# Optimization experiments

Measured on AMD Instinct MI355X. Metric: run time of the kernel, lower is better.

## Reference

```python
import jax, jax.numpy as jnp
import numpy as np

B = 2048
F = 267          # frame_size
L = 32           # latent_size
H = 256          # hidden_size (hard-coded in module)
E = 8            # num_experts
G = 64           # gate hidden size (hard-coded)
IN0 = L + F      # decoder layer0 input (latent + frame*cond_frames)
IN1 = L + H      # decoder inter input
OUT = F          # num_future_predictions * frame_size


def _lin_init(key, out_dim, in_dim):
    # kaiming-uniform-like scale
    bound = float(np.sqrt(1.0 / in_dim))
    return jax.random.uniform(key, (out_dim, in_dim), jnp.float32, -bound, bound)


def setup_inputs() -> dict:
    key = jax.random.key(0)
    ks = jax.random.split(key, 24)
    d = {}
    d["x"] = jax.random.normal(ks[0], (B, F), jnp.float32)
    d["c"] = jax.random.normal(ks[1], (B, F), jnp.float32)
    # encoder
    d["fc1_w"] = _lin_init(ks[2], H, 2 * F); d["fc1_b"] = jnp.zeros((H,), jnp.float32)
    d["fc2_w"] = _lin_init(ks[3], H, F + H); d["fc2_b"] = jnp.zeros((H,), jnp.float32)
    d["mu_w"] = _lin_init(ks[4], L, F + H);  d["mu_b"] = jnp.zeros((L,), jnp.float32)
    d["lv_w"] = _lin_init(ks[5], L, F + H);  d["lv_b"] = jnp.zeros((L,), jnp.float32)
    # gate
    d["g0_w"] = _lin_init(ks[6], G, IN0); d["g0_b"] = jnp.zeros((G,), jnp.float32)
    d["g1_w"] = _lin_init(ks[7], G, G);   d["g1_b"] = jnp.zeros((G,), jnp.float32)
    d["g2_w"] = _lin_init(ks[8], E, G);   d["g2_b"] = jnp.zeros((E,), jnp.float32)
    # expert weights [E, in, out], biases [E, out], bias filled 0.01 as in module
    d["w0"] = jax.random.uniform(ks[9], (E, IN0, H), jnp.float32, -1, 1) * np.sqrt(1.0 / IN0)
    d["b0"] = jnp.full((E, H), 0.01, jnp.float32)
    d["w1"] = jax.random.uniform(ks[10], (E, IN1, H), jnp.float32, -1, 1) * np.sqrt(1.0 / IN1)
    d["b1"] = jnp.full((E, H), 0.01, jnp.float32)
    d["w2"] = jax.random.uniform(ks[11], (E, IN1, OUT), jnp.float32, -1, 1) * np.sqrt(1.0 / IN1)
    d["b2"] = jnp.full((E, OUT), 0.01, jnp.float32)
    return d


def reference(x, c, fc1_w, fc1_b, fc2_w, fc2_b, mu_w, mu_b, lv_w, lv_b,
              g0_w, g0_b, g1_w, g1_b, g2_w, g2_b, w0, b0, w1, b1, w2, b2):
    elu = jax.nn.elu
    # ---- encoder ----
    h1 = elu(jnp.concatenate([x, c], axis=1) @ fc1_w.T + fc1_b)
    h2 = elu(jnp.concatenate([x, h1], axis=1) @ fc2_w.T + fc2_b)
    s = jnp.concatenate([x, h2], axis=1)
    mu = s @ mu_w.T + mu_b
    logvar = s @ lv_w.T + lv_b
    eps = jax.random.normal(jax.random.key(42), mu.shape, mu.dtype)
    z = mu + eps * jnp.exp(0.5 * logvar)
    # ---- mixed decoder ----
    g = elu(jnp.concatenate([z, c], axis=1) @ g0_w.T + g0_b)
    g = elu(g @ g1_w.T + g1_b)
    coeff = jax.nn.softmax(g @ g2_w.T + g2_b, axis=1)  # [B, E]
    layer_out = c
    for (W, bvec, act) in ((w0, b0, True), (w1, b1, True), (w2, b2, False)):
        inp = jnp.concatenate([z, layer_out], axis=1)          # [B, in]
        # per-expert GEMM then coefficient mixing (same math as per-sample
        # mixed-weight bmm: coeff @ flat_weight then baddbmm)
        out = jnp.einsum('be,bi,eio->bo', coeff, inp, W, optimize=True)
        out = out + coeff @ bvec                               # mixed bias
        layer_out = elu(out) if act else out
    return (layer_out, mu, logvar)
```

## Files before the change

### kernel.cpp

```cpp
#include <hip/hip_runtime.h>
#include <math.h>
#include <stdint.h>

#define DI __device__ __forceinline__

typedef __attribute__((ext_vector_type(8))) short bf16x8;
typedef __attribute__((ext_vector_type(4))) float f32x4;
typedef __attribute__((ext_vector_type(4))) int i32x4;

DI float elu_f(float v) { return v > 0.f ? v : expm1f(v); }

DI unsigned short f2bf(float f) {
  uint32_t u = __float_as_uint(f);
  return (unsigned short)((u + 0x7FFFu + ((u >> 16) & 1u)) >> 16);
}

DI void threefry2x32(uint32_t k0, uint32_t k1, uint32_t& x0, uint32_t& x1) {
  uint32_t ks0 = k0, ks1 = k1, ks2 = k0 ^ k1 ^ 0x1BD11BDAu;
  x0 += ks0; x1 += ks1;
#define TFR(r) { x0 += x1; x1 = (x1 << r) | (x1 >> (32 - r)); x1 ^= x0; }
  TFR(13) TFR(15) TFR(26) TFR(6)   x0 += ks1; x1 += ks2 + 1u;
  TFR(17) TFR(29) TFR(16) TFR(24)  x0 += ks2; x1 += ks0 + 2u;
  TFR(13) TFR(15) TFR(26) TFR(6)   x0 += ks0; x1 += ks1 + 3u;
  TFR(17) TFR(29) TFR(16) TFR(24)  x0 += ks1; x1 += ks2 + 4u;
  TFR(13) TFR(15) TFR(26) TFR(6)   x0 += ks2; x1 += ks0 + 5u;
#undef TFR
}

DI float erfinv_f(float x) {
  float w = -logf((1.0f - x) * (1.0f + x));
  float p;
  if (w < 5.0f) {
    w -= 2.5f;
    p = 2.81022636e-08f;
    p = fmaf(p, w, 3.43273939e-07f);
    p = fmaf(p, w, -3.5233877e-06f);
    p = fmaf(p, w, -4.39150654e-06f);
    p = fmaf(p, w, 0.00021858087f);
    p = fmaf(p, w, -0.00125372503f);
    p = fmaf(p, w, -0.00417768164f);
    p = fmaf(p, w, 0.246640727f);
    p = fmaf(p, w, 1.50140941f);
  } else {
    w = sqrtf(w) - 3.0f;
    p = -0.000200214257f;
    p = fmaf(p, w, 0.000100950558f);
    p = fmaf(p, w, 0.00134934322f);
    p = fmaf(p, w, -0.00367342844f);
    p = fmaf(p, w, 0.00573950773f);
    p = fmaf(p, w, -0.0076224613f);
    p = fmaf(p, w, 0.00943887047f);
    p = fmaf(p, w, 1.00167406f);
    p = fmaf(p, w, 2.83297682f);
  }
  return p * x;
}

struct MegaArgs {
  const float *x, *c;
  const float *fc1w, *fc1b, *fc2w, *fc2b, *muw, *mub, *lvw, *lvb;
  const float *g0w, *g0b, *g1w, *g1b, *g2w, *g2b;
  const float *w0, *b0, *w1, *b1, *w2, *b2;
  unsigned short *Ax, *Axh, *Axh2, *A0, *A1, *A2;
  unsigned short *fc1t, *fc2t, *mlvt, *g0t, *g1t, *w0b, *w1b, *w2b;
  float *cf, *outY, *outMu, *outLv;
};

template <int KT, int NE, int D, bool ELU, bool OUTF32>
__global__ __launch_bounds__(128, 2)
void pipe32(const unsigned short* __restrict__ A,
            const unsigned short* __restrict__ Wt, int N,
            const float* __restrict__ bias,
            const float* __restrict__ cfp,
            unsigned short* __restrict__ Cb, int ldcb, int cb_off,
            float* __restrict__ Cf) {
  constexpr int Kp = KT * 32, TT = NE * KT;
  __shared__ float bias_s[NE * 32];
  __shared__ float cfs[(NE > 1) ? 256 : 1];
  const int tid = threadIdx.x, lane = tid & 63, wv = tid >> 6;
  const int q = lane >> 4, l16 = lane & 15;
  const int m0 = blockIdx.x * 32;
  const int n0 = blockIdx.y * 32 + wv * 16;
  const int gc = n0 + l16;
  const int wrow = (gc < N) ? gc : (N - 1);
  const unsigned short* wlane = Wt + (size_t)wrow * Kp + q * 8;

  bf16x8 ring[D];
#pragma unroll
  for (int g = 0; g < D; g++) {
    if (g < TT) {
      int e = g / KT, c = g % KT;
      ring[g] = *(const bf16x8*)(wlane + (size_t)e * N * Kp + c * 32);
    }
  }
  bf16x8 areg[2][KT];
#pragma unroll
  for (int t = 0; t < 2; t++) {
    const unsigned short* alane = A + (size_t)(m0 + t * 16 + l16) * Kp + q * 8;
#pragma unroll
    for (int c = 0; c < KT; c++) areg[t][c] = *(const bf16x8*)(alane + c * 32);
  }

  if (NE == 1) {
    if (tid < 32) {
      int col = blockIdx.y * 32 + tid;
      bias_s[tid] = (col < N) ? bias[col] : 0.f;
    }
  } else {
    for (int idx = tid; idx < NE * 32; idx += 128) {
      int e = idx >> 5, col = blockIdx.y * 32 + (idx & 31);
      bias_s[idx] = (col < N) ? bias[(size_t)e * N + col] : 0.f;
    }
    for (int idx = tid; idx < 256; idx += 128)
      cfs[idx] = cfp[(size_t)(m0 + (idx >> 3)) * 8 + (idx & 7)];
  }
  __syncthreads();

  f32x4 acc[2] = {{0.f, 0.f, 0.f, 0.f}, {0.f, 0.f, 0.f, 0.f}};
  f32x4 accF[2] = {{0.f, 0.f, 0.f, 0.f}, {0.f, 0.f, 0.f, 0.f}};
#pragma unroll
  for (int g = 0; g < TT; g++) {
    const int e = g / KT, c = g % KT;
    bf16x8 bv = ring[g % D];
    acc[0] = __builtin_amdgcn_mfma_f32_16x16x32_bf16(areg[0][c], bv, acc[0], 0, 0, 0);
    acc[1] = __builtin_amdgcn_mfma_f32_16x16x32_bf16(areg[1][c], bv, acc[1], 0, 0, 0);
    if (g + D < TT) {
      int e2 = (g + D) / KT, c2 = (g + D) % KT;
      ring[g % D] = *(const bf16x8*)(wlane + (size_t)e2 * N * Kp + c2 * 32);
    }
    if (NE > 1 && c == KT - 1) {
      float bv2 = bias_s[e * 32 + wv * 16 + l16];
#pragma unroll
      for (int t = 0; t < 2; t++)
#pragma unroll
        for (int r = 0; r < 4; r++) {
          float ce = cfs[(t * 16 + q * 4 + r) * 8 + e];
          accF[t][r] += ce * (acc[t][r] + bv2);
          acc[t][r] = 0.f;
        }
    }
  }

  if (gc < N) {
#pragma unroll
    for (int t = 0; t < 2; t++)
#pragma unroll
      for (int r = 0; r < 4; r++) {
        int row = m0 + t * 16 + q * 4 + r;
        float v = (NE > 1) ? accF[t][r] : (acc[t][r] + bias_s[wv * 16 + l16]);
        if (ELU) v = elu_f(v);
        if (OUTF32) Cf[(size_t)row * 267 + gc] = v;
        else Cb[(size_t)row * ldcb + cb_off + gc] = f2bf(v);
      }
  }
}

__global__ __launch_bounds__(256) void k_prep(MegaArgs a) {
  __shared__ __align__(16) unsigned short T[64][72];
  const int bb = blockIdx.x, tid = threadIdx.x;
  if (bb < 512) {
    for (int rr = 0; rr < 4; rr++) {
      int b = bb * 4 + rr;
      const float* xr = a.x + (size_t)b * 267;
      const float* cr = a.c + (size_t)b * 267;
      unsigned short* axr = a.Ax + (size_t)b * 544;
      for (int k = tid; k < 544; k += 256) {
        float v = (k < 267) ? xr[k] : ((k < 534) ? cr[k - 267] : 0.f);
        axr[k] = f2bf(v);
      }
      unsigned short* ahr = a.Axh + (size_t)b * 544;
      unsigned short* ah2 = a.Axh2 + (size_t)b * 544;
      for (int k = tid; k < 267; k += 256) { unsigned short v = f2bf(xr[k]); ahr[k] = v; ah2[k] = v; }
      for (int k = 523 + tid; k < 544; k += 256) { ahr[k] = 0; ah2[k] = 0; }
      unsigned short* a0r = a.A0 + (size_t)b * 320;
      for (int k = tid; k < 288; k += 256)
        a0r[32 + k] = (k < 267) ? f2bf(cr[k]) : (unsigned short)0;
    }
  } else if (bb < 1152) {
    int r = bb - 512;
    const float* src; unsigned short* dst; int Ks, Kp2;
    if (r < 256)      { src = a.fc1w + (size_t)r * 534; dst = a.fc1t + (size_t)r * 544; Ks = 534; Kp2 = 544; }
    else if (r < 512) { int n = r - 256; src = a.fc2w + (size_t)n * 523; dst = a.fc2t + (size_t)n * 544; Ks = 523; Kp2 = 544; }
    else if (r < 576) { int n = r - 512; src = (n < 32) ? (a.muw + (size_t)n * 523) : (a.lvw + (size_t)(n - 32) * 523);
                        dst = a.mlvt + (size_t)n * 544; Ks = 523; Kp2 = 544; }
    else              { int n = r - 576; src = a.g0w + (size_t)n * 299; dst = a.g0t + (size_t)n * 320; Ks = 299; Kp2 = 320; }
    for (int k = tid; k < Kp2; k += 256) dst[k] = (k < Ks) ? f2bf(src[k]) : (unsigned short)0;
  } else if (bb == 1152) {
    for (int k = tid; k < 4096; k += 256) a.g1t[k] = f2bf(a.g1w[k]);
  } else {
    int t = bb - 1153;
    const float* W; unsigned short* D; int K, N2, Kp2, ldW, e, kt, nt;
    if (t < 160)      { e = t / 20;  int lt = t % 20;  kt = lt / 4; nt = lt % 4; W = a.w0; D = a.w0b; K = 299; N2 = 256; Kp2 = 320; ldW = 256; }
    else if (t < 320) { int u = t - 160; e = u / 20; int lt = u % 20; kt = lt / 4; nt = lt % 4; W = a.w1; D = a.w1b; K = 288; N2 = 256; Kp2 = 288; ldW = 256; }
    else              { int u = t - 320; e = u / 25; int lt = u % 25; kt = lt / 5; nt = lt % 5; W = a.w2; D = a.w2b; K = 288; N2 = 267; Kp2 = 288; ldW = 267; }
    const int k0 = kt * 64, n0 = nt * 64;
    const float* We = W + (size_t)e * K * ldW;
    const int jj = tid & 63, ii0 = tid >> 6;
#pragma unroll
    for (int p = 0; p < 16; p++) {
      int i = ii0 + p * 4;
      int gk = k0 + i, gn = n0 + jj;
      float v = (gk < K && gn < N2) ? We[(size_t)gk * ldW + gn] : 0.f;
      T[jj][i] = f2bf(v);
    }
    __syncthreads();
    int j = tid >> 2, chb = tid & 3;
    int gn = n0 + j;
    if (gn < N2) {
      unsigned short* drow = D + ((size_t)e * N2 + gn) * Kp2 + k0;
#pragma unroll
      for (int s = 0; s < 2; s++) {
        int ch = chb + s * 4;
        if (k0 + ch * 8 < Kp2) {
          i32x4 v = *(i32x4*)(&T[j][ch * 8]);
          *(i32x4*)(drow + ch * 8) = v;
        }
      }
    }
  }
}

__global__ __launch_bounds__(256, 2) void k_mulv_gate(MegaArgs a) {
  __shared__ float mlvS[16 * 65];
  __shared__ __align__(16) unsigned short A0p[16 * 328];
  __shared__ __align__(16) unsigned short gaB[16 * 72];
  __shared__ __align__(16) unsigned short g1B[64 * 72];
  __shared__ float g2wT[64 * 8];
  __shared__ float gB[16 * 65];
  __shared__ float lg[16 * 8];
  const int tid = threadIdx.x, lane = tid & 63, wid = tid >> 6;
  const int q = lane >> 4, l16 = lane & 15;
  const int m0 = blockIdx.x * 16;
  const int cl = wid * 16 + l16;

  const unsigned short* alane = a.Axh2 + (size_t)(m0 + l16) * 544 + q * 8;
  const unsigned short* wlA = a.mlvt + (size_t)cl * 544 + q * 8;
  bf16x8 ring[8];
#pragma unroll
  for (int g = 0; g < 8; g++) ring[g] = *(const bf16x8*)(wlA + g * 32);
  bf16x8 areg[17];
#pragma unroll
  for (int c = 0; c < 17; c++) areg[c] = *(const bf16x8*)(alane + c * 32);
  f32x4 acc = {0.f, 0.f, 0.f, 0.f};
#pragma unroll
  for (int g = 0; g < 17; g++) {
    acc = __builtin_amdgcn_mfma_f32_16x16x32_bf16(areg[g], ring[g % 8], acc, 0, 0, 0);
    if (g + 8 < 17) ring[g % 8] = *(const bf16x8*)(wlA + (g + 8) * 32);
  }
#pragma unroll
  for (int r = 0; r < 4; r++) mlvS[(q * 4 + r) * 65 + cl] = acc[r];
  for (int idx = tid; idx < 576; idx += 256) {
    int row = idx / 36, ch = 4 + idx % 36;
    *(i32x4*)(A0p + row * 328 + ch * 8) =
        *(const i32x4*)(a.A0 + (size_t)(m0 + row) * 320 + ch * 8);
  }
  if (tid < 16) { i32x4 z4 = {0, 0, 0, 0}; *(i32x4*)(A0p + tid * 328 + 320) = z4; }
  for (int idx = tid; idx < 512; idx += 256) {
    int row = idx >> 3, ch = idx & 7;
    *(i32x4*)(g1B + row * 72 + ch * 8) = *(const i32x4*)(a.g1t + (size_t)row * 64 + ch * 8);
  }
  for (int idx = tid; idx < 512; idx += 256)
    g2wT[(idx & 63) * 8 + (idx >> 6)] = a.g2w[idx];
  __syncthreads();

  {
    const int m = tid >> 4, j0 = (tid & 15) * 2, R = m0 + m;
#pragma unroll
    for (int jj = 0; jj < 2; jj++) {
      int j = j0 + jj;
      float mu = mlvS[m * 65 + j] + a.mub[j];
      float lvv = mlvS[m * 65 + j + 32] + a.lvb[j];
      uint32_t x0 = 0u, x1 = (uint32_t)(R * 32 + j);
      threefry2x32(0u, 42u, x0, x1);
      uint32_t bits = x0 ^ x1;
      float f = __uint_as_float((bits >> 9) | 0x3F800000u) - 1.0f;
      const float lo = -0.99999994039535522461f;
      float u = fmaf(f, 2.0f, lo);
      u = fmaxf(u, lo);
      float eps = 1.41421356237f * erfinv_f(u);
      float z = fmaf(eps, expf(0.5f * lvv), mu);
      a.outMu[(size_t)R * 32 + j] = mu;
      a.outLv[(size_t)R * 32 + j] = lvv;
      unsigned short zb = f2bf(z);
      A0p[m * 328 + j] = zb;
      a.A0[(size_t)R * 320 + j] = zb;
      a.A1[(size_t)R * 288 + j] = zb;
      a.A2[(size_t)R * 288 + j] = zb;
    }
  }
  __syncthreads();

  const unsigned short* wlC = a.g0t + (size_t)cl * 320 + q * 8;
  bf16x8 ring2[8];
#pragma unroll
  for (int g = 0; g < 8; g++) ring2[g] = *(const bf16x8*)(wlC + g * 32);
  f32x4 accC = {0.f, 0.f, 0.f, 0.f};
#pragma unroll
  for (int g = 0; g < 10; g++) {
    bf16x8 av = *(const bf16x8*)(A0p + l16 * 328 + g * 32 + q * 8);
    accC = __builtin_amdgcn_mfma_f32_16x16x32_bf16(av, ring2[g % 8], accC, 0, 0, 0);
    if (g + 8 < 10) ring2[g % 8] = *(const bf16x8*)(wlC + (g + 8) * 32);
  }
  {
    float bc = a.g0b[cl];
#pragma unroll
    for (int r = 0; r < 4; r++)
      gaB[(q * 4 + r) * 72 + cl] = f2bf(elu_f(accC[r] + bc));
  }
  __syncthreads();

  f32x4 accD = {0.f, 0.f, 0.f, 0.f};
#pragma unroll
  for (int tau = 0; tau < 2; tau++) {
    bf16x8 av = *(const bf16x8*)(gaB + l16 * 72 + tau * 32 + q * 8);
    bf16x8 bv = *(const bf16x8*)(g1B + cl * 72 + tau * 32 + q * 8);
    accD = __builtin_amdgcn_mfma_f32_16x16x32_bf16(av, bv, accD, 0, 0, 0);
  }
  {
    float bc = a.g1b[cl];
#pragma unroll
    for (int r = 0; r < 4; r++)
      gB[(q * 4 + r) * 65 + cl] = elu_f(accD[r] + bc);
  }
  __syncthreads();

  if (tid < 128) {
    int r = tid >> 3, e = tid & 7;
    float d = a.g2b[e];
#pragma unroll 8
    for (int k = 0; k < 64; k++) d = fmaf(gB[r * 65 + k], g2wT[k * 8 + e], d);
    lg[r * 8 + e] = d;
  }
  __syncthreads();
  if (tid < 16) {
    float mx = lg[tid * 8];
#pragma unroll
    for (int e2 = 1; e2 < 8; e2++) mx = fmaxf(mx, lg[tid * 8 + e2]);
    float s = 0.f, ex[8];
#pragma unroll
    for (int e2 = 0; e2 < 8; e2++) { ex[e2] = expf(lg[tid * 8 + e2] - mx); s += ex[e2]; }
    float inv = 1.f / s;
#pragma unroll
    for (int e2 = 0; e2 < 8; e2++) a.cf[(size_t)(m0 + tid) * 8 + e2] = ex[e2] * inv;
  }
}

extern "C" void kernel_launch(void* const* d_in, const int* in_sizes, int n_in,
                              void* d_out, int out_size, void* d_ws, size_t ws_size,
                              hipStream_t stream) {
  (void)in_sizes; (void)n_in; (void)out_size; (void)ws_size;
  float* out = (float*)d_out;
  float* ws = (float*)d_ws;

  MegaArgs a;
  a.x    = (const float*)d_in[0];
  a.c    = (const float*)d_in[1];
  a.fc1w = (const float*)d_in[2];  a.fc1b = (const float*)d_in[3];
  a.fc2w = (const float*)d_in[4];  a.fc2b = (const float*)d_in[5];
  a.muw  = (const float*)d_in[6];  a.mub  = (const float*)d_in[7];
  a.lvw  = (const float*)d_in[8];  a.lvb  = (const float*)d_in[9];
  a.g0w  = (const float*)d_in[10]; a.g0b  = (const float*)d_in[11];
  a.g1w  = (const float*)d_in[12]; a.g1b  = (const float*)d_in[13];
  a.g2w  = (const float*)d_in[14]; a.g2b  = (const float*)d_in[15];
  a.w0   = (const float*)d_in[16]; a.b0   = (const float*)d_in[17];
  a.w1   = (const float*)d_in[18]; a.b1   = (const float*)d_in[19];
  a.w2   = (const float*)d_in[20]; a.b2   = (const float*)d_in[21];

  a.outY  = out;
  a.outMu = out + 2048 * 267;
  a.outLv = a.outMu + 2048 * 32;

  a.Ax   = (unsigned short*)(ws);
  a.Axh  = (unsigned short*)(ws + 557056);
  a.Axh2 = (unsigned short*)(ws + 1114112);
  a.A0   = (unsigned short*)(ws + 1671168);
  a.A1   = (unsigned short*)(ws + 1998848);
  a.A2   = (unsigned short*)(ws + 2293760);
  a.fc1t = (unsigned short*)(ws + 2588672);
  a.fc2t = (unsigned short*)(ws + 2658304);
  a.mlvt = (unsigned short*)(ws + 2727936);
  a.g0t  = (unsigned short*)(ws + 2745344);
  a.g1t  = (unsigned short*)(ws + 2755584);
  a.w0b  = (unsigned short*)(ws + 2757632);
  a.w1b  = (unsigned short*)(ws + 3085312);
  a.w2b  = (unsigned short*)(ws + 3380224);
  a.cf   = ws + 3687808;

  dim3 blkP(256), blkG(128);
  k_prep<<<1673, blkP, 0, stream>>>(a);
  pipe32<17, 1, 12, true, false><<<dim3(64, 8), blkG, 0, stream>>>(
      a.Ax, a.fc1t, 256, a.fc1b, nullptr, a.Axh, 544, 267, nullptr);
  pipe32<17, 1, 12, true, false><<<dim3(64, 8), blkG, 0, stream>>>(
      a.Axh, a.fc2t, 256, a.fc2b, nullptr, a.Axh2, 544, 267, nullptr);
  k_mulv_gate<<<128, blkP, 0, stream>>>(a);
  pipe32<10, 8, 12, true, false><<<dim3(64, 8), blkG, 0, stream>>>(
      a.A0, a.w0b, 256, a.b0, a.cf, a.A1, 288, 32, nullptr);
  pipe32<9, 8, 12, true, false><<<dim3(64, 8), blkG, 0, stream>>>(
      a.A1, a.w1b, 256, a.b1, a.cf, a.A2, 288, 32, nullptr);
  pipe32<9, 8, 12, false, true><<<dim3(64, 9), blkG, 0, stream>>>(
      a.A2, a.w2b, 267, a.b2, a.cf, nullptr, 0, 0, a.outY);
}
```

Measured before the change: 175.8 us.

## Fuse prep into encoder GEMMs and convert fp32 weights to bf16 on the fly

Removes the separate prep kernel. The first encoder GEMM now loads x/c fp32 rows directly into LDS as bf16 and writes the x part of the next activation buffer. The expert weight transposes run as extra blocks of that same launch. Encoder, mu/logvar and gate GEMMs read fp32 weights directly and pack them to bf16 in registers, which removes the transposed-weight buffers and one launch. The cost is more global fp32 weight traffic per block, with strided per-lane scalar loads and redundant conversion work in every block.

```diff
diff --git a/kernel.cpp b/kernel.cpp
--- a/kernel.cpp
+++ b/kernel.cpp
@@ -8,11 +8,20 @@
 typedef __attribute__((ext_vector_type(4))) float f32x4;
 typedef __attribute__((ext_vector_type(4))) int i32x4;
 
+#define MFMA16(av, bv, acc) __builtin_amdgcn_mfma_f32_16x16x32_bf16(av, bv, acc, 0, 0, 0)
+
 DI float elu_f(float v) { return v > 0.f ? v : expm1f(v); }
 
 DI unsigned short f2bf(float f) {
   uint32_t u = __float_as_uint(f);
   return (unsigned short)((u + 0x7FFFu + ((u >> 16) & 1u)) >> 16);
+}
+
+DI bf16x8 pack8(const float (&v)[8]) {
+  bf16x8 o;
+#pragma unroll
+  for (int j = 0; j < 8; j++) o[j] = (short)f2bf(v[j]);
+  return o;
 }
 
 DI void threefry2x32(uint32_t k0, uint32_t k1, uint32_t& x0, uint32_t& x1) {
@@ -61,150 +70,33 @@
   const float *fc1w, *fc1b, *fc2w, *fc2b, *muw, *mub, *lvw, *lvb;
   const float *g0w, *g0b, *g1w, *g1b, *g2w, *g2b;
   const float *w0, *b0, *w1, *b1, *w2, *b2;
-  unsigned short *Ax, *Axh, *Axh2, *A0, *A1, *A2;
-  unsigned short *fc1t, *fc2t, *mlvt, *g0t, *g1t, *w0b, *w1b, *w2b;
+  unsigned short *Axh, *Axh2, *A0, *A1, *A2;
+  unsigned short *w0b, *w1b, *w2b;
   float *cf, *outY, *outMu, *outLv;
 };
 
-template <int KT, int NE, int D, bool ELU, bool OUTF32>
-__global__ __launch_bounds__(128, 2)
-void pipe32(const unsigned short* __restrict__ A,
-            const unsigned short* __restrict__ Wt, int N,
-            const float* __restrict__ bias,
-            const float* __restrict__ cfp,
-            unsigned short* __restrict__ Cb, int ldcb, int cb_off,
-            float* __restrict__ Cf) {
-  constexpr int Kp = KT * 32, TT = NE * KT;
-  __shared__ float bias_s[NE * 32];
-  __shared__ float cfs[(NE > 1) ? 256 : 1];
-  const int tid = threadIdx.x, lane = tid & 63, wv = tid >> 6;
-  const int q = lane >> 4, l16 = lane & 15;
-  const int m0 = blockIdx.x * 32;
-  const int n0 = blockIdx.y * 32 + wv * 16;
-  const int gc = n0 + l16;
-  const int wrow = (gc < N) ? gc : (N - 1);
-  const unsigned short* wlane = Wt + (size_t)wrow * Kp + q * 8;
-
-  bf16x8 ring[D];
-#pragma unroll
-  for (int g = 0; g < D; g++) {
-    if (g < TT) {
-      int e = g / KT, c = g % KT;
-      ring[g] = *(const bf16x8*)(wlane + (size_t)e * N * Kp + c * 32);
-    }
-  }
-  bf16x8 areg[2][KT];
-#pragma unroll
-  for (int t = 0; t < 2; t++) {
-    const unsigned short* alane = A + (size_t)(m0 + t * 16 + l16) * Kp + q * 8;
-#pragma unroll
-    for (int c = 0; c < KT; c++) areg[t][c] = *(const bf16x8*)(alane + c * 32);
-  }
-
-  if (NE == 1) {
-    if (tid < 32) {
-      int col = blockIdx.y * 32 + tid;
-      bias_s[tid] = (col < N) ? bias[col] : 0.f;
-    }
-  } else {
-    for (int idx = tid; idx < NE * 32; idx += 128) {
-      int e = idx >> 5, col = blockIdx.y * 32 + (idx & 31);
-      bias_s[idx] = (col < N) ? bias[(size_t)e * N + col] : 0.f;
-    }
-    for (int idx = tid; idx < 256; idx += 128)
-      cfs[idx] = cfp[(size_t)(m0 + (idx >> 3)) * 8 + (idx & 7)];
-  }
-  __syncthreads();
-
-  f32x4 acc[2] = {{0.f, 0.f, 0.f, 0.f}, {0.f, 0.f, 0.f, 0.f}};
-  f32x4 accF[2] = {{0.f, 0.f, 0.f, 0.f}, {0.f, 0.f, 0.f, 0.f}};
-#pragma unroll
-  for (int g = 0; g < TT; g++) {
-    const int e = g / KT, c = g % KT;
-    bf16x8 bv = ring[g % D];
-    acc[0] = __builtin_amdgcn_mfma_f32_16x16x32_bf16(areg[0][c], bv, acc[0], 0, 0, 0);
-    acc[1] = __builtin_amdgcn_mfma_f32_16x16x32_bf16(areg[1][c], bv, acc[1], 0, 0, 0);
-    if (g + D < TT) {
-      int e2 = (g + D) / KT, c2 = (g + D) % KT;
-      ring[g % D] = *(const bf16x8*)(wlane + (size_t)e2 * N * Kp + c2 * 32);
-    }
-    if (NE > 1 && c == KT - 1) {
-      float bv2 = bias_s[e * 32 + wv * 16 + l16];
-#pragma unroll
-      for (int t = 0; t < 2; t++)
-#pragma unroll
-        for (int r = 0; r < 4; r++) {
-          float ce = cfs[(t * 16 + q * 4 + r) * 8 + e];
-          accF[t][r] += ce * (acc[t][r] + bv2);
-          acc[t][r] = 0.f;
-        }
-    }
-  }
-
-  if (gc < N) {
-#pragma unroll
-    for (int t = 0; t < 2; t++)
-#pragma unroll
-      for (int r = 0; r < 4; r++) {
-        int row = m0 + t * 16 + q * 4 + r;
-        float v = (NE > 1) ? accF[t][r] : (acc[t][r] + bias_s[wv * 16 + l16]);
-        if (ELU) v = elu_f(v);
-        if (OUTF32) Cf[(size_t)row * 267 + gc] = v;
-        else Cb[(size_t)row * ldcb + cb_off + gc] = f2bf(v);
-      }
-  }
-}
-
-__global__ __launch_bounds__(256) void k_prep(MegaArgs a) {
-  __shared__ __align__(16) unsigned short T[64][72];
-  const int bb = blockIdx.x, tid = threadIdx.x;
-  if (bb < 512) {
-    for (int rr = 0; rr < 4; rr++) {
-      int b = bb * 4 + rr;
-      const float* xr = a.x + (size_t)b * 267;
-      const float* cr = a.c + (size_t)b * 267;
-      unsigned short* axr = a.Ax + (size_t)b * 544;
-      for (int k = tid; k < 544; k += 256) {
-        float v = (k < 267) ? xr[k] : ((k < 534) ? cr[k - 267] : 0.f);
-        axr[k] = f2bf(v);
-      }
-      unsigned short* ahr = a.Axh + (size_t)b * 544;
-      unsigned short* ah2 = a.Axh2 + (size_t)b * 544;
-      for (int k = tid; k < 267; k += 256) { unsigned short v = f2bf(xr[k]); ahr[k] = v; ah2[k] = v; }
-      for (int k = 523 + tid; k < 544; k += 256) { ahr[k] = 0; ah2[k] = 0; }
-      unsigned short* a0r = a.A0 + (size_t)b * 320;
-      for (int k = tid; k < 288; k += 256)
-        a0r[32 + k] = (k < 267) ? f2bf(cr[k]) : (unsigned short)0;
-    }
-  } else if (bb < 1152) {
-    int r = bb - 512;
-    const float* src; unsigned short* dst; int Ks, Kp2;
-    if (r < 256)      { src = a.fc1w + (size_t)r * 534; dst = a.fc1t + (size_t)r * 544; Ks = 534; Kp2 = 544; }
-    else if (r < 512) { int n = r - 256; src = a.fc2w + (size_t)n * 523; dst = a.fc2t + (size_t)n * 544; Ks = 523; Kp2 = 544; }
-    else if (r < 576) { int n = r - 512; src = (n < 32) ? (a.muw + (size_t)n * 523) : (a.lvw + (size_t)(n - 32) * 523);
-                        dst = a.mlvt + (size_t)n * 544; Ks = 523; Kp2 = 544; }
-    else              { int n = r - 576; src = a.g0w + (size_t)n * 299; dst = a.g0t + (size_t)n * 320; Ks = 299; Kp2 = 320; }
-    for (int k = tid; k < Kp2; k += 256) dst[k] = (k < Ks) ? f2bf(src[k]) : (unsigned short)0;
-  } else if (bb == 1152) {
-    for (int k = tid; k < 4096; k += 256) a.g1t[k] = f2bf(a.g1w[k]);
-  } else {
-    int t = bb - 1153;
-    const float* W; unsigned short* D; int K, N2, Kp2, ldW, e, kt, nt;
-    if (t < 160)      { e = t / 20;  int lt = t % 20;  kt = lt / 4; nt = lt % 4; W = a.w0; D = a.w0b; K = 299; N2 = 256; Kp2 = 320; ldW = 256; }
-    else if (t < 320) { int u = t - 160; e = u / 20; int lt = u % 20; kt = lt / 4; nt = lt % 4; W = a.w1; D = a.w1b; K = 288; N2 = 256; Kp2 = 288; ldW = 256; }
-    else              { int u = t - 320; e = u / 25; int lt = u % 25; kt = lt / 5; nt = lt % 5; W = a.w2; D = a.w2b; K = 288; N2 = 267; Kp2 = 288; ldW = 267; }
-    const int k0 = kt * 64, n0 = nt * 64;
-    const float* We = W + (size_t)e * K * ldW;
-    const int jj = tid & 63, ii0 = tid >> 6;
-#pragma unroll
-    for (int p = 0; p < 16; p++) {
-      int i = ii0 + p * 4;
-      int gk = k0 + i, gn = n0 + jj;
-      float v = (gk < K && gn < N2) ? We[(size_t)gk * ldW + gn] : 0.f;
-      T[jj][i] = f2bf(v);
-    }
-    __syncthreads();
-    int j = tid >> 2, chb = tid & 3;
+DI void transpose_job(unsigned char* smemv, int t, const MegaArgs& a) {
+  unsigned short (*T)[72] = (unsigned short (*)[72])smemv;
+  const int tid = threadIdx.x;
+  const float* W; unsigned short* D; int K, N2, Kp2, ldW, e, kt, nt;
+  if (t < 160)      { e = t / 20;  int lt = t % 20;  kt = lt / 4; nt = lt % 4; W = a.w0; D = a.w0b; K = 299; N2 = 256; Kp2 = 320; ldW = 256; }
+  else if (t < 320) { int u = t - 160; e = u / 20; int lt = u % 20; kt = lt / 4; nt = lt % 4; W = a.w1; D = a.w1b; K = 288; N2 = 256; Kp2 = 288; ldW = 256; }
+  else              { int u = t - 320; e = u / 25; int lt = u % 25; kt = lt / 5; nt = lt % 5; W = a.w2; D = a.w2b; K = 288; N2 = 267; Kp2 = 288; ldW = 267; }
+  const int k0 = kt * 64, n0 = nt * 64;
+  const float* We = W + (size_t)e * K * ldW;
+  const int jj = tid & 63, ii0 = tid >> 6;
+#pragma unroll
+  for (int p = 0; p < 32; p++) {
+    int i = ii0 + p * 2;
+    int gk = k0 + i, gn = n0 + jj;
+    float v = (gk < K && gn < N2) ? We[(size_t)gk * ldW + gn] : 0.f;
+    T[jj][i] = f2bf(v);
+  }
+  __syncthreads();
+  const int j0 = tid >> 2, chb = tid & 3;
+#pragma unroll
+  for (int jh = 0; jh < 2; jh++) {
+    int j = j0 + jh * 32;
     int gn = n0 + j;
     if (gn < N2) {
       unsigned short* drow = D + ((size_t)e * N2 + gn) * Kp2 + k0;
@@ -218,6 +110,89 @@
       }
     }
   }
+}
+
+template <int KS, bool FIRST>
+DI void enc_gemm(unsigned char* smemv, int bid, const MegaArgs& a,
+                 const float* __restrict__ Wf, const float* __restrict__ bias,
+                 const unsigned short* __restrict__ Aprev,
+                 unsigned short* __restrict__ Aout) {
+  unsigned short (*sA)[552] = (unsigned short (*)[552])smemv;
+  const int tid = threadIdx.x, lane = tid & 63, wv = tid >> 6;
+  const int q = lane >> 4, l16 = lane & 15;
+  const int bx = bid & 63, by = bid >> 6;
+  const int m0 = bx * 32;
+  const int gc = by * 32 + wv * 16 + l16;
+
+  if (FIRST) {
+    for (int r = 0; r < 32; r++) {
+      const float* xr = a.x + (size_t)(m0 + r) * 267;
+      const float* cr = a.c + (size_t)(m0 + r) * 267;
+      for (int k = tid; k < 544; k += 128) {
+        float v = (k < 267) ? xr[k] : ((k < 534) ? cr[k - 267] : 0.f);
+        sA[r][k] = f2bf(v);
+      }
+    }
+  } else {
+    for (int idx = tid; idx < 32 * 68; idx += 128) {
+      int r = idx / 68, ch = idx % 68;
+      *(i32x4*)(&sA[r][ch * 8]) =
+          *(const i32x4*)(Aprev + (size_t)(m0 + r) * 544 + ch * 8);
+    }
+  }
+  __syncthreads();
+
+  const float* wrowp = Wf + (size_t)gc * KS;
+  float rf[8][8];
+#pragma unroll
+  for (int g = 0; g < 8; g++)
+#pragma unroll
+    for (int j = 0; j < 8; j++) rf[g][j] = wrowp[g * 32 + q * 8 + j];
+
+  f32x4 acc0 = {0.f, 0.f, 0.f, 0.f}, acc1 = {0.f, 0.f, 0.f, 0.f};
+#pragma unroll
+  for (int g = 0; g < 17; g++) {
+    bf16x8 bv = pack8(rf[g & 7]);
+    bf16x8 av0 = *(const bf16x8*)(&sA[l16][g * 32 + q * 8]);
+    bf16x8 av1 = *(const bf16x8*)(&sA[16 + l16][g * 32 + q * 8]);
+    acc0 = MFMA16(av0, bv, acc0);
+    acc1 = MFMA16(av1, bv, acc1);
+    if (g + 8 < 17) {
+#pragma unroll
+      for (int j = 0; j < 8; j++) {
+        int k = (g + 8) * 32 + q * 8 + j;
+        rf[g & 7][j] = wrowp[(k < KS) ? k : (KS - 1)];
+      }
+    }
+  }
+
+  float bc = bias[gc];
+#pragma unroll
+  for (int r = 0; r < 4; r++) {
+    Aout[(size_t)(m0 + q * 4 + r) * 544 + 267 + gc] = f2bf(elu_f(acc0[r] + bc));
+    Aout[(size_t)(m0 + 16 + q * 4 + r) * 544 + 267 + gc] = f2bf(elu_f(acc1[r] + bc));
+  }
+
+  if (by == 0) {
+    for (int idx = tid; idx < 32 * 288; idx += 128) {
+      int r = idx / 288, k = idx % 288;
+      int col = (k < 267) ? k : (k + 256);
+      Aout[(size_t)(m0 + r) * 544 + col] = (k < 267) ? sA[r][k] : (unsigned short)0;
+    }
+  }
+}
+
+__global__ __launch_bounds__(128, 2) void k_d1(MegaArgs a) {
+  __shared__ __align__(16) unsigned char smem[32 * 552 * 2];
+  if (blockIdx.x < 512)
+    enc_gemm<534, true>(smem, blockIdx.x, a, a.fc1w, a.fc1b, nullptr, a.Axh);
+  else
+    transpose_job(smem, blockIdx.x - 512, a);
+}
+
+__global__ __launch_bounds__(128, 2) void k_d2(MegaArgs a) {
+  __shared__ __align__(16) unsigned char smem[32 * 552 * 2];
+  enc_gemm<523, false>(smem, blockIdx.x, a, a.fc2w, a.fc2b, a.Axh, a.Axh2);
 }
 
 __global__ __launch_bounds__(256, 2) void k_mulv_gate(MegaArgs a) {
@@ -234,31 +209,41 @@
   const int cl = wid * 16 + l16;
 
   const unsigned short* alane = a.Axh2 + (size_t)(m0 + l16) * 544 + q * 8;
-  const unsigned short* wlA = a.mlvt + (size_t)cl * 544 + q * 8;
-  bf16x8 ring[8];
-#pragma unroll
-  for (int g = 0; g < 8; g++) ring[g] = *(const bf16x8*)(wlA + g * 32);
+  const float* wrow = (cl < 32) ? (a.muw + (size_t)cl * 523)
+                                : (a.lvw + (size_t)(cl - 32) * 523);
+  float rf[4][8];
+#pragma unroll
+  for (int g = 0; g < 4; g++)
+#pragma unroll
+    for (int j = 0; j < 8; j++) rf[g][j] = wrow[g * 32 + q * 8 + j];
   bf16x8 areg[17];
 #pragma unroll
   for (int c = 0; c < 17; c++) areg[c] = *(const bf16x8*)(alane + c * 32);
   f32x4 acc = {0.f, 0.f, 0.f, 0.f};
 #pragma unroll
   for (int g = 0; g < 17; g++) {
-    acc = __builtin_amdgcn_mfma_f32_16x16x32_bf16(areg[g], ring[g % 8], acc, 0, 0, 0);
-    if (g + 8 < 17) ring[g % 8] = *(const bf16x8*)(wlA + (g + 8) * 32);
+    acc = MFMA16(areg[g], pack8(rf[g & 3]), acc);
+    if (g + 4 < 17) {
+#pragma unroll
+      for (int j = 0; j < 8; j++) {
+        int k = (g + 4) * 32 + q * 8 + j;
+        rf[g & 3][j] = wrow[(k < 523) ? k : 522];
+      }
+    }
   }
 #pragma unroll
   for (int r = 0; r < 4; r++) mlvS[(q * 4 + r) * 65 + cl] = acc[r];
-  for (int idx = tid; idx < 576; idx += 256) {
-    int row = idx / 36, ch = 4 + idx % 36;
-    *(i32x4*)(A0p + row * 328 + ch * 8) =
-        *(const i32x4*)(a.A0 + (size_t)(m0 + row) * 320 + ch * 8);
+
+  for (int idx = tid; idx < 16 * 288; idx += 256) {
+    int row = idx / 288, k = idx % 288;
+    unsigned short b = (k < 267) ? f2bf(a.c[(size_t)(m0 + row) * 267 + k])
+                                 : (unsigned short)0;
+    A0p[row * 328 + 32 + k] = b;
+    a.A0[(size_t)(m0 + row) * 320 + 32 + k] = b;
   }
   if (tid < 16) { i32x4 z4 = {0, 0, 0, 0}; *(i32x4*)(A0p + tid * 328 + 320) = z4; }
-  for (int idx = tid; idx < 512; idx += 256) {
-    int row = idx >> 3, ch = idx & 7;
-    *(i32x4*)(g1B + row * 72 + ch * 8) = *(const i32x4*)(a.g1t + (size_t)row * 64 + ch * 8);
-  }
+  for (int idx = tid; idx < 4096; idx += 256)
+    g1B[(idx >> 6) * 72 + (idx & 63)] = f2bf(a.g1w[idx]);
   for (int idx = tid; idx < 512; idx += 256)
     g2wT[(idx & 63) * 8 + (idx >> 6)] = a.g2w[idx];
   __syncthreads();
@@ -290,18 +275,26 @@
   }
   __syncthreads();
 
-  const unsigned short* wlC = a.g0t + (size_t)cl * 320 + q * 8;
-  bf16x8 ring2[8];
-#pragma unroll
-  for (int g = 0; g < 8; g++) ring2[g] = *(const bf16x8*)(wlC + g * 32);
-  f32x4 accC = {0.f, 0.f, 0.f, 0.f};
-#pragma unroll
-  for (int g = 0; g < 10; g++) {
-    bf16x8 av = *(const bf16x8*)(A0p + l16 * 328 + g * 32 + q * 8);
-    accC = __builtin_amdgcn_mfma_f32_16x16x32_bf16(av, ring2[g % 8], accC, 0, 0, 0);
-    if (g + 8 < 10) ring2[g % 8] = *(const bf16x8*)(wlC + (g + 8) * 32);
-  }
   {
+    const float* wrowC = a.g0w + (size_t)cl * 299;
+    float rf2[4][8];
+#pragma unroll
+    for (int g = 0; g < 4; g++)
+#pragma unroll
+      for (int j = 0; j < 8; j++) rf2[g][j] = wrowC[g * 32 + q * 8 + j];
+    f32x4 accC = {0.f, 0.f, 0.f, 0.f};
+#pragma unroll
+    for (int g = 0; g < 10; g++) {
+      bf16x8 av = *(const bf16x8*)(A0p + l16 * 328 + g * 32 + q * 8);
+      accC = MFMA16(av, pack8(rf2[g & 3]), accC);
+      if (g + 4 < 10) {
+#pragma unroll
+        for (int j = 0; j < 8; j++) {
+          int k = (g + 4) * 32 + q * 8 + j;
+          rf2[g & 3][j] = wrowC[(k < 299) ? k : 298];
+        }
+      }
+    }
     float bc = a.g0b[cl];
 #pragma unroll
     for (int r = 0; r < 4; r++)
@@ -314,7 +307,7 @@
   for (int tau = 0; tau < 2; tau++) {
     bf16x8 av = *(const bf16x8*)(gaB + l16 * 72 + tau * 32 + q * 8);
     bf16x8 bv = *(const bf16x8*)(g1B + cl * 72 + tau * 32 + q * 8);
-    accD = __builtin_amdgcn_mfma_f32_16x16x32_bf16(av, bv, accD, 0, 0, 0);
+    accD = MFMA16(av, bv, accD);
   }
   {
     float bc = a.g1b[cl];
@@ -345,12 +338,101 @@
   }
 }
 
+template <int KT, int NE, int D, bool ELU, bool OUTF32>
+__global__ __launch_bounds__(128, 2)
+void pipe32(const unsigned short* __restrict__ A,
+            const unsigned short* __restrict__ Wt, int N,
+            const float* __restrict__ bias,
+            const float* __restrict__ cfp,
+            unsigned short* __restrict__ Cb, int ldcb, int cb_off,
+            float* __restrict__ Cf) {
+  constexpr int Kp = KT * 32, TT = NE * KT;
+  __shared__ float bias_s[NE * 32];
+  __shared__ float cfs[(NE > 1) ? 256 : 1];
+  const int tid = threadIdx.x, lane = tid & 63, wv = tid >> 6;
+  const int q = lane >> 4, l16 = lane & 15;
+  const int m0 = blockIdx.x * 32;
+  const int n0 = blockIdx.y * 32 + wv * 16;
+  const int gc = n0 + l16;
+  const int wrow = (gc < N) ? gc : (N - 1);
+  const unsigned short* wlane = Wt + (size_t)wrow * Kp + q * 8;
+
+  bf16x8 ring[D];
+#pragma unroll
+  for (int g = 0; g < D; g++) {
+    if (g < TT) {
+      int e = g / KT, c = g % KT;
+      ring[g] = *(const bf16x8*)(wlane + (size_t)e * N * Kp + c * 32);
+    }
+  }
+  bf16x8 areg[2][KT];
+#pragma unroll
+  for (int t = 0; t < 2; t++) {
+    const unsigned short* alane = A + (size_t)(m0 + t * 16 + l16) * Kp + q * 8;
+#pragma unroll
+    for (int c = 0; c < KT; c++) areg[t][c] = *(const bf16x8*)(alane + c * 32);
+  }
+
+  if (NE == 1) {
+    if (tid < 32) {
+      int col = blockIdx.y * 32 + tid;
+      bias_s[tid] = (col < N) ? bias[col] : 0.f;
+    }
+  } else {
+    for (int idx = tid; idx < NE * 32; idx += 128) {
+      int e = idx >> 5, col = blockIdx.y * 32 + (idx & 31);
+      bias_s[idx] = (col < N) ? bias[(size_t)e * N + col] : 0.f;
+    }
+    for (int idx = tid; idx < 256; idx += 128)
+      cfs[idx] = cfp[(size_t)(m0 + (idx >> 3)) * 8 + (idx & 7)];
+  }
+  __syncthreads();
+
+  f32x4 acc[2] = {{0.f, 0.f, 0.f, 0.f}, {0.f, 0.f, 0.f, 0.f}};
+  f32x4 accF[2] = {{0.f, 0.f, 0.f, 0.f}, {0.f, 0.f, 0.f, 0.f}};
+#pragma unroll
+  for (int g = 0; g < TT; g++) {
+    const int e = g / KT, c = g % KT;
+    bf16x8 bv = ring[g % D];
+    acc[0] = MFMA16(areg[0][c], bv, acc[0]);
+    acc[1] = MFMA16(areg[1][c], bv, acc[1]);
+    if (g + D < TT) {
+      int e2 = (g + D) / KT, c2 = (g + D) % KT;
+      ring[g % D] = *(const bf16x8*)(wlane + (size_t)e2 * N * Kp + c2 * 32);
+    }
+    if (NE > 1 && c == KT - 1) {
+      float bv2 = bias_s[e * 32 + wv * 16 + l16];
+#pragma unroll
+      for (int t = 0; t < 2; t++)
+#pragma unroll
+        for (int r = 0; r < 4; r++) {
+          float ce = cfs[(t * 16 + q * 4 + r) * 8 + e];
+          accF[t][r] += ce * (acc[t][r] + bv2);
+          acc[t][r] = 0.f;
+        }
+    }
+  }
+
+  if (gc < N) {
+#pragma unroll
+    for (int t = 0; t < 2; t++)
+#pragma unroll
+      for (int r = 0; r < 4; r++) {
+        int row = m0 + t * 16 + q * 4 + r;
+        float v = (NE > 1) ? accF[t][r] : (acc[t][r] + bias_s[wv * 16 + l16]);
+        if (ELU) v = elu_f(v);
+        if (OUTF32) Cf[(size_t)row * 267 + gc] = v;
+        else Cb[(size_t)row * ldcb + cb_off + gc] = f2bf(v);
+      }
+  }
+}
+
 extern "C" void kernel_launch(void* const* d_in, const int* in_sizes, int n_in,
                               void* d_out, int out_size, void* d_ws, size_t ws_size,
                               hipStream_t stream) {
   (void)in_sizes; (void)n_in; (void)out_size; (void)ws_size;
   float* out = (float*)d_out;
-  float* ws = (float*)d_ws;
+  char* ws = (char*)d_ws;
 
   MegaArgs a;
   a.x    = (const float*)d_in[0];
@@ -370,33 +452,23 @@
   a.outMu = out + 2048 * 267;
   a.outLv = a.outMu + 2048 * 32;
 
-  a.Ax   = (unsigned short*)(ws);
-  a.Axh  = (unsigned short*)(ws + 557056);
-  a.Axh2 = (unsigned short*)(ws + 1114112);
-  a.A0   = (unsigned short*)(ws + 1671168);
-  a.A1   = (unsigned short*)(ws + 1998848);
-  a.A2   = (unsigned short*)(ws + 2293760);
-  a.fc1t = (unsigned short*)(ws + 2588672);
-  a.fc2t = (unsigned short*)(ws + 2658304);
-  a.mlvt = (unsigned short*)(ws + 2727936);
-  a.g0t  = (unsigned short*)(ws + 2745344);
-  a.g1t  = (unsigned short*)(ws + 2755584);
-  a.w0b  = (unsigned short*)(ws + 2757632);
-  a.w1b  = (unsigned short*)(ws + 3085312);
-  a.w2b  = (unsigned short*)(ws + 3380224);
-  a.cf   = ws + 3687808;
-
-  dim3 blkP(256), blkG(128);
-  k_prep<<<1673, blkP, 0, stream>>>(a);
-  pipe32<17, 1, 12, true, false><<<dim3(64, 8), blkG, 0, stream>>>(
-      a.Ax, a.fc1t, 256, a.fc1b, nullptr, a.Axh, 544, 267, nullptr);
-  pipe32<17, 1, 12, true, false><<<dim3(64, 8), blkG, 0, stream>>>(
-      a.Axh, a.fc2t, 256, a.fc2b, nullptr, a.Axh2, 544, 267, nullptr);
-  k_mulv_gate<<<128, blkP, 0, stream>>>(a);
-  pipe32<10, 8, 12, true, false><<<dim3(64, 8), blkG, 0, stream>>>(
+  a.Axh  = (unsigned short*)(ws + 0);
+  a.Axh2 = (unsigned short*)(ws + 2228224);
+  a.A0   = (unsigned short*)(ws + 4456448);
+  a.A1   = (unsigned short*)(ws + 5767168);
+  a.A2   = (unsigned short*)(ws + 6946816);
+  a.w0b  = (unsigned short*)(ws + 8126464);
+  a.w1b  = (unsigned short*)(ws + 9437184);
+  a.w2b  = (unsigned short*)(ws + 10616832);
+  a.cf   = (float*)(ws + 11847168);
+
+  k_d1<<<1032, 128, 0, stream>>>(a);
+  k_d2<<<512, 128, 0, stream>>>(a);
+  k_mulv_gate<<<128, 256, 0, stream>>>(a);
+  pipe32<10, 8, 12, true, false><<<dim3(64, 8), 128, 0, stream>>>(
       a.A0, a.w0b, 256, a.b0, a.cf, a.A1, 288, 32, nullptr);
-  pipe32<9, 8, 12, true, false><<<dim3(64, 8), blkG, 0, stream>>>(
+  pipe32<9, 8, 12, true, false><<<dim3(64, 8), 128, 0, stream>>>(
       a.A1, a.w1b, 256, a.b1, a.cf, a.A2, 288, 32, nullptr);
-  pipe32<9, 8, 12, false, true><<<dim3(64, 9), blkG, 0, stream>>>(
+  pipe32<9, 8, 12, false, true><<<dim3(64, 9), 128, 0, stream>>>(
       a.A2, a.w2b, 267, a.b2, a.cf, nullptr, 0, 0, a.outY);
 }
```

Measured after the change: 235.8 us. +34.1%, slower.
